# Optimization experiments

Hardware: AMD Instinct MI355X
Metric: run time of the kernel (lower is better)

The kernel has to match this reference:

```python
import jax, jax.numpy as jnp
import numpy as np

N = 100000      # nodes
E = 3200000     # directed edges
G = 1024        # graphs in batch


def setup_inputs() -> dict:
    key = jax.random.key(0)
    ks = jax.random.split(key, 12)
    x = jax.random.normal(ks[0], (N, 4), dtype=jnp.float32)
    edge_index = jax.random.randint(ks[1], (2, E), 0, N, dtype=jnp.int64)
    batch = jnp.sort(jax.random.randint(ks[2], (N,), 0, G, dtype=jnp.int64))
    s = 0.1
    return {
        'x': x, 'edge_index': edge_index, 'batch': batch,
        'W_emb': jax.random.normal(ks[3], (4, 1), jnp.float32) * s,
        'b_emb': jax.random.normal(ks[4], (4,), jnp.float32) * s,
        'W1': jax.random.normal(ks[5], (16, 7), jnp.float32) * s,
        'b1': jax.random.normal(ks[6], (16,), jnp.float32) * s,
        'W2': jax.random.normal(ks[7], (8, 16), jnp.float32) * s,
        'b2': jax.random.normal(ks[8], (8,), jnp.float32) * s,
        'W3': jax.random.normal(ks[9], (1, 8), jnp.float32) * s,
        'b3': jax.random.normal(ks[10], (1,), jnp.float32) * s,
    }


def _gcn_norm(edge_index, n):
    # add self-loops (PyG GCNConv default)
    loops = jnp.arange(n, dtype=edge_index.dtype)
    row = jnp.concatenate([edge_index[0], loops])  # source
    col = jnp.concatenate([edge_index[1], loops])  # target
    deg = jax.ops.segment_sum(jnp.ones_like(col, dtype=jnp.float32), col, num_segments=n)
    dinv = jnp.where(deg > 0, deg ** -0.5, 0.0)
    norm = dinv[row] * dinv[col]
    return row, col, norm


def _gcn_conv(h, W, b, row, col, norm, n):
    h = h @ W.T                                   # [n, out]
    msg = h[row] * norm[:, None]                  # gather + scale
    out = jax.ops.segment_sum(msg, col, num_segments=n)
    return out + b


def reference(x, edge_index, batch, W_emb, b_emb, W1, b1, W2, b2, W3, b3):
    row, col, norm = _gcn_norm(edge_index, N)
    atoms_vector = x[:, :1]
    atoms_xyz = x[:, 1:]
    one_hot_emb = atoms_vector @ W_emb.T + b_emb          # [N, 4]
    h = jnp.concatenate([one_hot_emb, atoms_xyz], axis=1) # [N, 7]
    h = jnp.tanh(_gcn_conv(h, W1, b1, row, col, norm, N)) # [N, 16]
    # dropout is identity in eval mode
    h = jnp.tanh(_gcn_conv(h, W2, b2, row, col, norm, N)) # [N, 8]
    # scatter-mean readout over graphs
    sums = jax.ops.segment_sum(h, batch, num_segments=G)
    cnts = jax.ops.segment_sum(jnp.ones((h.shape[0],), h.dtype), batch, num_segments=G)
    pooled = sums / jnp.maximum(cnts, 1.0)[:, None]       # [G, 8]
    return pooled @ W3.T + b3                             # [G, 1]
```

## Files before the change

### kernel.cpp

```cpp
#include <hip/hip_runtime.h>
#include <hip/hip_fp16.h>


constexpr int BLK  = 256;
constexpr int NPB  = 256;
constexpr int NBMX = 512;
constexpr int CAPB = 9216;
constexpr int PBLK = 512;
constexpr int CAPS = 6144;
constexpr int EPT  = 12;
constexpr int SBLK = 512;
constexpr int NIT4 = 5;
constexpr float S8 = 64.0f;

__global__ void k_place(const int4* __restrict__ row4, const int4* __restrict__ col4,
                        int* __restrict__ bucketCnt, unsigned int* __restrict__ data,
                        int E, int NB) {
    __shared__ unsigned int stage[CAPS];
    __shared__ unsigned short stageB[CAPS];
    __shared__ int pos[4][NBMX];
    __shared__ int sstart[NBMX], lbase[NBMX];
    __shared__ int wsum[8];
    int t = threadIdx.x;
    int lane = t & 63, w = t >> 6;
    int rep = (lane >> 4) & 3;
    int begin = blockIdx.x * CAPS;
    int end = min(E, begin + CAPS);
    int csize = end - begin;
    int q0 = begin >> 2, q1 = end >> 2;
#pragma unroll
    for (int rr = 0; rr < 4; rr++) pos[rr][t] = 0;
    __syncthreads();
    unsigned int ent[EPT];
    int meta[EPT];
#pragma unroll
    for (int it = 0; it < EPT / 4; it++) {
        int i = q0 + t + it * PBLK;
        bool ok = i < q1;
        int4 c = ok ? col4[i] : make_int4(0, 0, 0, 0);
        int4 r = ok ? row4[i] : make_int4(0, 0, 0, 0);
#pragma unroll
        for (int k = 0; k < 4; k++) {
            int cc = ((const int*)&c)[k];
            int rr = ((const int*)&r)[k];
            int b = cc >> 8;
            int o = ok ? atomicAdd(&pos[rep][b], 1) : 0;
            ent[it * 4 + k] = ((unsigned int)(cc & 255) << 17) | (unsigned int)rr;
            meta[it * 4 + k] = ok ? ((rep << 22) | (b << 13) | o) : -1;
        }
    }
    __syncthreads();
    int p0 = pos[0][t], p1 = pos[1][t], p2 = pos[2][t], p3 = pos[3][t];
    int v = p0 + p1 + p2 + p3;
    int sc = v;
#pragma unroll
    for (int off = 1; off < 64; off <<= 1) {
        int o = __shfl_up(sc, off, 64);
        if (lane >= off) sc += o;
    }
    if (lane == 63) wsum[w] = sc;
    __syncthreads();
    int pre = 0;
#pragma unroll
    for (int i = 0; i < 8; i++) if (i < w) pre += wsum[i];
    int excl = sc + pre - v;
    sstart[t] = excl;
    lbase[t] = v ? atomicAdd(&bucketCnt[t], v) : 0;
    pos[0][t] = 0;
    pos[1][t] = p0;
    pos[2][t] = p0 + p1;
    pos[3][t] = p0 + p1 + p2;
    __syncthreads();
#pragma unroll
    for (int k = 0; k < EPT; k++) {
        int m = meta[k];
        if (m >= 0) {
            int rr = m >> 22;
            int b  = (m >> 13) & 0x1FF;
            int o  = m & 0x1FFF;
            int idx = sstart[b] + pos[rr][b] + o;
            stage[idx]  = ent[k];
            stageB[idx] = (unsigned short)b;
        }
    }
    __syncthreads();
    for (int k = t; k < csize; k += PBLK) {
        int b = stageB[k];
        data[(unsigned int)b * CAPB + (unsigned int)(lbase[b] + (k - sstart[b]))] = stage[k];
    }
}

__global__ void k_sort_node1(unsigned int* __restrict__ data,
                             const int* __restrict__ bucketCnt,
                             const float4* __restrict__ x,
                             const float* __restrict__ Wemb, const float* __restrict__ bemb,
                             const float* __restrict__ W1,
                             int* __restrict__ rs, int* __restrict__ re,
                             float* __restrict__ dinv, uint4* __restrict__ u1q, int n) {
    __shared__ int pos[8][NPB], startl[NPB];
    __shared__ int wsum[4];
    int b = blockIdx.x;
    int t = threadIdx.x;
    int lane = t & 63;
    int rep = (lane >> 3) & 7;
    int base = b * CAPB;
    int cnt = min(bucketCnt[b], CAPB);
#pragma unroll
    for (int z = 0; z < 4; z++) ((int*)pos)[t + z * SBLK] = 0;
    __syncthreads();
    const uint4* data4 = (const uint4*)(data + base);
    unsigned int ent[NIT4 * 4];
    int off[NIT4 * 4];
#pragma unroll
    for (int it = 0; it < NIT4; it++) {
        int i4 = t + it * SBLK;
        int i = i4 * 4;
        uint4 p4 = (i < cnt) ? data4[i4] : make_uint4(0, 0, 0, 0);
#pragma unroll
        for (int k = 0; k < 4; k++) {
            int idx = it * 4 + k;
            if (i + k < cnt) {
                unsigned int p = ((const unsigned int*)&p4)[k];
                int dloc = (int)(p >> 17);
                int o = atomicAdd(&pos[rep][dloc], 1);
                ent[idx] = p & 0x1FFFF;
                off[idx] = (rep << 22) | (dloc << 14) | o;
            } else off[idx] = -1;
        }
    }
    __syncthreads();
    int node = b * NPB + t;
    float d = 0.0f;
    if (t < NPB) {
        int w = t >> 6;
        int p[8];
        int v = 0;
#pragma unroll
        for (int r = 0; r < 8; r++) { p[r] = pos[r][t]; v += p[r]; }
        int sc = v;
#pragma unroll
        for (int o = 1; o < 64; o <<= 1) {
            int s = __shfl_up(sc, o, 64);
            if (lane >= o) sc += s;
        }
        if (lane == 63) wsum[w] = sc;
        __syncthreads();
        int pre = 0;
#pragma unroll
        for (int i = 0; i < 4; i++) if (i < w) pre += wsum[i];
        int excl = sc + pre - v;
        startl[t] = excl;
        int run = 0;
#pragma unroll
        for (int r = 0; r < 8; r++) { pos[r][t] = run; run += p[r]; }
        if (node < n) {
            rs[node] = base + excl;
            re[node] = base + excl + v;
            d = rsqrtf((float)v + 1.0f);
            dinv[node] = d;
        }
    } else {
        __syncthreads();
    }
    __syncthreads();
#pragma unroll
    for (int it = 0; it < NIT4 * 4; it++) {
        int m = off[it];
        if (m >= 0) {
            int rr = (m >> 22) & 7;
            int dl = (m >> 14) & 255;
            int o  = m & 0x3FFF;
            data[base + startl[dl] + pos[rr][dl] + o] = ent[it];
        }
    }
    if (t < NPB && node < n) {
        float4 xi = x[node];
        float h0[7];
#pragma unroll
        for (int j = 0; j < 4; j++) h0[j] = xi.x * Wemb[j] + bemb[j];
        h0[4] = xi.y; h0[5] = xi.z; h0[6] = xi.w;
        float s[16];
#pragma unroll
        for (int f = 0; f < 16; f++) {
            float tt = 0.0f;
#pragma unroll
            for (int j = 0; j < 7; j++) tt += h0[j] * W1[f * 7 + j];
            s[f] = tt * d * S8;
        }
        unsigned int w0, w1, w2, w3;
        w0 = __builtin_amdgcn_cvt_pk_fp8_f32(s[0],  s[1],  0,  false);
        w0 = __builtin_amdgcn_cvt_pk_fp8_f32(s[2],  s[3],  w0, true);
        w1 = __builtin_amdgcn_cvt_pk_fp8_f32(s[4],  s[5],  0,  false);
        w1 = __builtin_amdgcn_cvt_pk_fp8_f32(s[6],  s[7],  w1, true);
        w2 = __builtin_amdgcn_cvt_pk_fp8_f32(s[8],  s[9],  0,  false);
        w2 = __builtin_amdgcn_cvt_pk_fp8_f32(s[10], s[11], w2, true);
        w3 = __builtin_amdgcn_cvt_pk_fp8_f32(s[12], s[13], 0,  false);
        w3 = __builtin_amdgcn_cvt_pk_fp8_f32(s[14], s[15], w3, true);
        u1q[node] = make_uint4(w0, w1, w2, w3);
    }
}

typedef float vfloat2 __attribute__((vector_size(8)));

__device__ __forceinline__ void dec16_add(uint4 q, float* acc) {
#pragma unroll
    for (int w = 0; w < 4; w++) {
        unsigned int u = ((const unsigned int*)&q)[w];
        vfloat2 lo = __builtin_amdgcn_cvt_pk_f32_fp8(u, false);
        vfloat2 hi = __builtin_amdgcn_cvt_pk_f32_fp8(u, true);
        acc[4 * w + 0] += lo[0]; acc[4 * w + 1] += lo[1];
        acc[4 * w + 2] += hi[0]; acc[4 * w + 3] += hi[1];
    }
}

__global__ void k_agg1(const unsigned int* __restrict__ sorted,
                       const int* __restrict__ rs, const int* __restrict__ re,
                       const uint4* __restrict__ u1q, const float* __restrict__ dinv,
                       const float* __restrict__ b1, const float* __restrict__ W2,
                       uint4* __restrict__ u2q, int n) {
    int tt = blockIdx.x * BLK + threadIdx.x;
    int node = tt >> 2;
    int j = tt & 3;
    if (node >= n) return;
    int s = rs[node], e = re[node];
    float d = dinv[node];
    uint4 qs = make_uint4(0, 0, 0, 0);
    if (j == 0) qs = u1q[node];
    float acc[16];
#pragma unroll
    for (int k = 0; k < 16; k++) acc[k] = 0.0f;
    int i = s + j;
    for (; i + 12 < e; i += 16) {
        uint4 q0 = u1q[sorted[i]];
        uint4 q1 = u1q[sorted[i + 4]];
        uint4 q2 = u1q[sorted[i + 8]];
        uint4 q3 = u1q[sorted[i + 12]];
        dec16_add(q0, acc);
        dec16_add(q1, acc);
        dec16_add(q2, acc);
        dec16_add(q3, acc);
    }
    for (; i + 4 < e; i += 8) {
        uint4 q0 = u1q[sorted[i]];
        uint4 q1 = u1q[sorted[i + 4]];
        dec16_add(q0, acc);
        dec16_add(q1, acc);
    }
    if (i < e) {
        uint4 q = u1q[sorted[i]];
        dec16_add(q, acc);
    }
    if (j == 0) dec16_add(qs, acc);
#pragma unroll
    for (int k = 0; k < 16; k++) {
        acc[k] += __shfl_xor(acc[k], 1, 64);
        acc[k] += __shfl_xor(acc[k], 2, 64);
    }
    float dS = d * (1.0f / S8);
    float h1[16];
#pragma unroll
    for (int k = 0; k < 16; k++) h1[k] = tanhf(dS * acc[k] + b1[k]);
    float r[8];
#pragma unroll
    for (int g = 0; g < 8; g++) {
        float ttv = 0.0f;
#pragma unroll
        for (int k = 0; k < 16; k++) ttv += h1[k] * W2[g * 16 + k];
        r[g] = ttv * d;
    }
    if (j == 0) {
        union { __half2 h2[4]; uint4 u4; } pk;
#pragma unroll
        for (int q = 0; q < 4; q++) pk.h2[q] = __floats2half2_rn(r[2 * q], r[2 * q + 1]);
        u2q[node] = pk.u4;
    }
}

__device__ __forceinline__ void h16_add(uint4 q, float* acc) {
    const __half2* p = (const __half2*)&q;
#pragma unroll
    for (int k = 0; k < 4; k++) {
        float2 a = __half22float2(p[k]);
        acc[2 * k]     += a.x;
        acc[2 * k + 1] += a.y;
    }
}

__global__ void k_agg2_pool(const unsigned int* __restrict__ sorted,
                            const int* __restrict__ rs, const int* __restrict__ re,
                            const uint4* __restrict__ u2q, const float* __restrict__ dinv,
                            const float* __restrict__ b2, const int* __restrict__ batch,
                            float* __restrict__ pooled, float* __restrict__ cnt, int n) {
    int tt = blockIdx.x * BLK + threadIdx.x;
    int node = tt >> 2;
    int j = tt & 3;
    int lane = threadIdx.x & 63;
    bool valid = node < n;
    float h[8];
#pragma unroll
    for (int k = 0; k < 8; k++) h[k] = 0.0f;
    int g = -1;
    float c = 0.0f;
    if (valid) {
        int s = rs[node], e = re[node];
        float d = dinv[node];
        uint4 qs = make_uint4(0, 0, 0, 0);
        int gq = 0;
        if (j == 0) {
            qs = u2q[node];
            gq = batch[node];
        }
        float acc[8];
#pragma unroll
        for (int k = 0; k < 8; k++) acc[k] = 0.0f;
        int i = s + j;
        for (; i + 12 < e; i += 16) {
            uint4 q0 = u2q[sorted[i]];
            uint4 q1 = u2q[sorted[i + 4]];
            uint4 q2 = u2q[sorted[i + 8]];
            uint4 q3 = u2q[sorted[i + 12]];
            h16_add(q0, acc);
            h16_add(q1, acc);
            h16_add(q2, acc);
            h16_add(q3, acc);
        }
        for (; i + 4 < e; i += 8) {
            uint4 q0 = u2q[sorted[i]];
            uint4 q1 = u2q[sorted[i + 4]];
            h16_add(q0, acc);
            h16_add(q1, acc);
        }
        if (i < e) {
            uint4 q = u2q[sorted[i]];
            h16_add(q, acc);
        }
        if (j == 0) h16_add(qs, acc);
#pragma unroll
        for (int k = 0; k < 8; k++) {
            acc[k] += __shfl_xor(acc[k], 1, 64);
            acc[k] += __shfl_xor(acc[k], 2, 64);
        }
        if (j == 0) {
#pragma unroll
            for (int k = 0; k < 8; k++) h[k] = tanhf(d * acc[k] + b2[k]);
            g = gq;
            c = 1.0f;
        }
    }
#pragma unroll
    for (int off = 4; off < 64; off <<= 1) {
        int gn = __shfl_down(g, off, 64);
        float cn = __shfl_down(c, off, 64);
        float hn[8];
#pragma unroll
        for (int k = 0; k < 8; k++) hn[k] = __shfl_down(h[k], off, 64);
        bool take = (lane + off < 64) && (gn == g);
        if (take) {
            c += cn;
#pragma unroll
            for (int k = 0; k < 8; k++) h[k] += hn[k];
        }
    }
    int gprev = __shfl_up(g, 4, 64);
    bool head = valid && (j == 0) && (lane == 0 || gprev != g);
    if (head) {
#pragma unroll
        for (int k = 0; k < 8; k++) atomicAdd(&pooled[g * 8 + k], h[k]);
        atomicAdd(&cnt[g], c);
    }
}

__global__ void k_out(const float* __restrict__ pooled, const float* __restrict__ cnt,
                      const float* __restrict__ W3, const float* __restrict__ b3,
                      float* __restrict__ out, int G) {
    int g = blockIdx.x * BLK + threadIdx.x;
    if (g >= G) return;
    float c = fmaxf(cnt[g], 1.0f);
    float t = 0.0f;
#pragma unroll
    for (int k = 0; k < 8; k++) t += pooled[g * 8 + k] * W3[k];
    out[g] = t / c + b3[0];
}

extern "C" void kernel_launch(void* const* d_in, const int* in_sizes, int n_in,
                              void* d_out, int out_size, void* d_ws, size_t ws_size,
                              hipStream_t stream) {
    const float* x    = (const float*)d_in[0];
    const int*   ei   = (const int*)d_in[1];
    const int*   batch= (const int*)d_in[2];
    const float* Wemb = (const float*)d_in[3];
    const float* bemb = (const float*)d_in[4];
    const float* W1   = (const float*)d_in[5];
    const float* b1   = (const float*)d_in[6];
    const float* W2   = (const float*)d_in[7];
    const float* b2   = (const float*)d_in[8];
    const float* W3   = (const float*)d_in[9];
    const float* b3   = (const float*)d_in[10];
    float* out = (float*)d_out;

    const int n = in_sizes[2];
    const int E = in_sizes[1] / 2;
    const int G = out_size;
    const int* row = ei;
    const int* col = ei + E;
    const int NB = (n + NPB - 1) / NPB;

    float* ws    = (float*)d_ws;
    float* dinv  = ws;
    uint4* u1q   = (uint4*)(ws + n);
    __half* u2h  = (__half*)(ws + 9 * n);
    int* rs      = (int*)(ws + 13 * n);
    int* re      = rs + n;
    int* bucketCnt = re + n;
    float* pooled  = (float*)(bucketCnt + NBMX);
    float* cnt     = pooled + 8 * G;
    unsigned int* data = (unsigned int*)(cnt + G);

    int gridP = (E + CAPS - 1) / CAPS;
    int gridA = (4 * n + BLK - 1) / BLK;

    hipMemsetAsync(bucketCnt, 0, (NBMX + 8 * G + G) * sizeof(int), stream);
    k_place<<<gridP, PBLK, 0, stream>>>((const int4*)row, (const int4*)col,
                                        bucketCnt, data, E, NB);
    k_sort_node1<<<NB, SBLK, 0, stream>>>(data, bucketCnt, (const float4*)x,
                                          Wemb, bemb, W1, rs, re, dinv, u1q, n);
    k_agg1<<<gridA, BLK, 0, stream>>>(data, rs, re, u1q,
                                      dinv, b1, W2, (uint4*)u2h, n);
    k_agg2_pool<<<gridA, BLK, 0, stream>>>(data, rs, re,
                                           (const uint4*)u2h, dinv, b2,
                                           batch, pooled, cnt, n);
    k_out<<<(G + BLK - 1) / BLK, BLK, 0, stream>>>(pooled, cnt, W3, b3, out, G);
}
```

Measured before the change: 180.3 us.

## Replace bucketed two-pass CSR sort with global atomic histogram and scatter

Replaces the LDS-staged bucket placement and per-bucket local sort with a plain counting sort: a global atomic degree histogram, a per-block scan that claims row offsets through an atomic cursor, and an atomic-cursor scatter of source indices into CSR order. This drops the shared-memory staging and the capacity-bounded bucket layout, so the code is simpler and no longer has a per-bucket overflow limit. In exchange it issues millions of global atomics on random addresses plus random scattered writes, and edge order within a row becomes nondeterministic. Blocks claim row ranges through the cursor in arbitrary order, so node ranges are no longer laid out in node order.

New measurement: 536.3 us. 2.97x slower.

```diff
diff --git a/kernel.cpp b/kernel.cpp
--- a/kernel.cpp
+++ b/kernel.cpp
@@ -3,201 +3,92 @@
 
 
 constexpr int BLK  = 256;
-constexpr int NPB  = 256;
-constexpr int NBMX = 512;
-constexpr int CAPB = 9216;
-constexpr int PBLK = 512;
-constexpr int CAPS = 6144;
-constexpr int EPT  = 12;
-constexpr int SBLK = 512;
-constexpr int NIT4 = 5;
 constexpr float S8 = 64.0f;
 
-__global__ void k_place(const int4* __restrict__ row4, const int4* __restrict__ col4,
-                        int* __restrict__ bucketCnt, unsigned int* __restrict__ data,
-                        int E, int NB) {
-    __shared__ unsigned int stage[CAPS];
-    __shared__ unsigned short stageB[CAPS];
-    __shared__ int pos[4][NBMX];
-    __shared__ int sstart[NBMX], lbase[NBMX];
-    __shared__ int wsum[8];
+__global__ void k_hist(const int4* __restrict__ col4, int* __restrict__ deg, int nq) {
+    int i = blockIdx.x * BLK + threadIdx.x;
+    if (i >= nq) return;
+    int4 c = col4[i];
+    atomicAdd(&deg[c.x], 1);
+    atomicAdd(&deg[c.y], 1);
+    atomicAdd(&deg[c.z], 1);
+    atomicAdd(&deg[c.w], 1);
+}
+
+__global__ void k_node1(const int* __restrict__ deg,
+                        const float4* __restrict__ x,
+                        const float* __restrict__ Wemb, const float* __restrict__ bemb,
+                        const float* __restrict__ W1,
+                        int* __restrict__ rs, int* __restrict__ re,
+                        int* __restrict__ cur, float* __restrict__ dinv,
+                        uint4* __restrict__ u1q, int* __restrict__ bucketCursor, int n) {
+    __shared__ int wsum[4];
+    __shared__ int sbase;
     int t = threadIdx.x;
+    int node = blockIdx.x * BLK + t;
     int lane = t & 63, w = t >> 6;
-    int rep = (lane >> 4) & 3;
-    int begin = blockIdx.x * CAPS;
-    int end = min(E, begin + CAPS);
-    int csize = end - begin;
-    int q0 = begin >> 2, q1 = end >> 2;
-#pragma unroll
-    for (int rr = 0; rr < 4; rr++) pos[rr][t] = 0;
-    __syncthreads();
-    unsigned int ent[EPT];
-    int meta[EPT];
-#pragma unroll
-    for (int it = 0; it < EPT / 4; it++) {
-        int i = q0 + t + it * PBLK;
-        bool ok = i < q1;
-        int4 c = ok ? col4[i] : make_int4(0, 0, 0, 0);
-        int4 r = ok ? row4[i] : make_int4(0, 0, 0, 0);
-#pragma unroll
-        for (int k = 0; k < 4; k++) {
-            int cc = ((const int*)&c)[k];
-            int rr = ((const int*)&r)[k];
-            int b = cc >> 8;
-            int o = ok ? atomicAdd(&pos[rep][b], 1) : 0;
-            ent[it * 4 + k] = ((unsigned int)(cc & 255) << 17) | (unsigned int)rr;
-            meta[it * 4 + k] = ok ? ((rep << 22) | (b << 13) | o) : -1;
-        }
-    }
-    __syncthreads();
-    int p0 = pos[0][t], p1 = pos[1][t], p2 = pos[2][t], p3 = pos[3][t];
-    int v = p0 + p1 + p2 + p3;
+    int v = (node < n) ? deg[node] : 0;
     int sc = v;
 #pragma unroll
-    for (int off = 1; off < 64; off <<= 1) {
-        int o = __shfl_up(sc, off, 64);
-        if (lane >= off) sc += o;
+    for (int o = 1; o < 64; o <<= 1) {
+        int s = __shfl_up(sc, o, 64);
+        if (lane >= o) sc += s;
     }
     if (lane == 63) wsum[w] = sc;
     __syncthreads();
     int pre = 0;
 #pragma unroll
-    for (int i = 0; i < 8; i++) if (i < w) pre += wsum[i];
-    int excl = sc + pre - v;
-    sstart[t] = excl;
-    lbase[t] = v ? atomicAdd(&bucketCnt[t], v) : 0;
-    pos[0][t] = 0;
-    pos[1][t] = p0;
-    pos[2][t] = p0 + p1;
-    pos[3][t] = p0 + p1 + p2;
+    for (int i = 0; i < 4; i++) if (i < w) pre += wsum[i];
+    int excl = pre + sc - v;
+    int total = wsum[0] + wsum[1] + wsum[2] + wsum[3];
+    if (t == 0) sbase = atomicAdd(bucketCursor, total);
     __syncthreads();
-#pragma unroll
-    for (int k = 0; k < EPT; k++) {
-        int m = meta[k];
-        if (m >= 0) {
-            int rr = m >> 22;
-            int b  = (m >> 13) & 0x1FF;
-            int o  = m & 0x1FFF;
-            int idx = sstart[b] + pos[rr][b] + o;
-            stage[idx]  = ent[k];
-            stageB[idx] = (unsigned short)b;
-        }
-    }
-    __syncthreads();
-    for (int k = t; k < csize; k += PBLK) {
-        int b = stageB[k];
-        data[(unsigned int)b * CAPB + (unsigned int)(lbase[b] + (k - sstart[b]))] = stage[k];
-    }
-}
-
-__global__ void k_sort_node1(unsigned int* __restrict__ data,
-                             const int* __restrict__ bucketCnt,
-                             const float4* __restrict__ x,
-                             const float* __restrict__ Wemb, const float* __restrict__ bemb,
-                             const float* __restrict__ W1,
-                             int* __restrict__ rs, int* __restrict__ re,
-                             float* __restrict__ dinv, uint4* __restrict__ u1q, int n) {
-    __shared__ int pos[8][NPB], startl[NPB];
-    __shared__ int wsum[4];
-    int b = blockIdx.x;
-    int t = threadIdx.x;
-    int lane = t & 63;
-    int rep = (lane >> 3) & 7;
-    int base = b * CAPB;
-    int cnt = min(bucketCnt[b], CAPB);
-#pragma unroll
-    for (int z = 0; z < 4; z++) ((int*)pos)[t + z * SBLK] = 0;
-    __syncthreads();
-    const uint4* data4 = (const uint4*)(data + base);
-    unsigned int ent[NIT4 * 4];
-    int off[NIT4 * 4];
-#pragma unroll
-    for (int it = 0; it < NIT4; it++) {
-        int i4 = t + it * SBLK;
-        int i = i4 * 4;
-        uint4 p4 = (i < cnt) ? data4[i4] : make_uint4(0, 0, 0, 0);
-#pragma unroll
-        for (int k = 0; k < 4; k++) {
-            int idx = it * 4 + k;
-            if (i + k < cnt) {
-                unsigned int p = ((const unsigned int*)&p4)[k];
-                int dloc = (int)(p >> 17);
-                int o = atomicAdd(&pos[rep][dloc], 1);
-                ent[idx] = p & 0x1FFFF;
-                off[idx] = (rep << 22) | (dloc << 14) | o;
-            } else off[idx] = -1;
-        }
-    }
-    __syncthreads();
-    int node = b * NPB + t;
-    float d = 0.0f;
-    if (t < NPB) {
-        int w = t >> 6;
-        int p[8];
-        int v = 0;
-#pragma unroll
-        for (int r = 0; r < 8; r++) { p[r] = pos[r][t]; v += p[r]; }
-        int sc = v;
-#pragma unroll
-        for (int o = 1; o < 64; o <<= 1) {
-            int s = __shfl_up(sc, o, 64);
-            if (lane >= o) sc += s;
-        }
-        if (lane == 63) wsum[w] = sc;
-        __syncthreads();
-        int pre = 0;
-#pragma unroll
-        for (int i = 0; i < 4; i++) if (i < w) pre += wsum[i];
-        int excl = sc + pre - v;
-        startl[t] = excl;
-        int run = 0;
-#pragma unroll
-        for (int r = 0; r < 8; r++) { pos[r][t] = run; run += p[r]; }
-        if (node < n) {
-            rs[node] = base + excl;
-            re[node] = base + excl + v;
-            d = rsqrtf((float)v + 1.0f);
-            dinv[node] = d;
-        }
-    } else {
-        __syncthreads();
-    }
-    __syncthreads();
-#pragma unroll
-    for (int it = 0; it < NIT4 * 4; it++) {
-        int m = off[it];
-        if (m >= 0) {
-            int rr = (m >> 22) & 7;
-            int dl = (m >> 14) & 255;
-            int o  = m & 0x3FFF;
-            data[base + startl[dl] + pos[rr][dl] + o] = ent[it];
-        }
-    }
-    if (t < NPB && node < n) {
-        float4 xi = x[node];
-        float h0[7];
-#pragma unroll
-        for (int j = 0; j < 4; j++) h0[j] = xi.x * Wemb[j] + bemb[j];
-        h0[4] = xi.y; h0[5] = xi.z; h0[6] = xi.w;
-        float s[16];
-#pragma unroll
-        for (int f = 0; f < 16; f++) {
-            float tt = 0.0f;
-#pragma unroll
-            for (int j = 0; j < 7; j++) tt += h0[j] * W1[f * 7 + j];
-            s[f] = tt * d * S8;
-        }
-        unsigned int w0, w1, w2, w3;
-        w0 = __builtin_amdgcn_cvt_pk_fp8_f32(s[0],  s[1],  0,  false);
-        w0 = __builtin_amdgcn_cvt_pk_fp8_f32(s[2],  s[3],  w0, true);
-        w1 = __builtin_amdgcn_cvt_pk_fp8_f32(s[4],  s[5],  0,  false);
-        w1 = __builtin_amdgcn_cvt_pk_fp8_f32(s[6],  s[7],  w1, true);
-        w2 = __builtin_amdgcn_cvt_pk_fp8_f32(s[8],  s[9],  0,  false);
-        w2 = __builtin_amdgcn_cvt_pk_fp8_f32(s[10], s[11], w2, true);
-        w3 = __builtin_amdgcn_cvt_pk_fp8_f32(s[12], s[13], 0,  false);
-        w3 = __builtin_amdgcn_cvt_pk_fp8_f32(s[14], s[15], w3, true);
-        u1q[node] = make_uint4(w0, w1, w2, w3);
-    }
+    if (node >= n) return;
+    int r0 = sbase + excl;
+    rs[node] = r0;
+    re[node] = r0 + v;
+    cur[node] = r0;
+    float d = rsqrtf((float)v + 1.0f);
+    dinv[node] = d;
+    float4 xi = x[node];
+    float h0[7];
+#pragma unroll
+    for (int j = 0; j < 4; j++) h0[j] = xi.x * Wemb[j] + bemb[j];
+    h0[4] = xi.y; h0[5] = xi.z; h0[6] = xi.w;
+    float s[16];
+#pragma unroll
+    for (int f = 0; f < 16; f++) {
+        float tt = 0.0f;
+#pragma unroll
+        for (int j = 0; j < 7; j++) tt += h0[j] * W1[f * 7 + j];
+        s[f] = tt * d * S8;
+    }
+    unsigned int w0, w1, w2, w3;
+    w0 = __builtin_amdgcn_cvt_pk_fp8_f32(s[0],  s[1],  0,  false);
+    w0 = __builtin_amdgcn_cvt_pk_fp8_f32(s[2],  s[3],  w0, true);
+    w1 = __builtin_amdgcn_cvt_pk_fp8_f32(s[4],  s[5],  0,  false);
+    w1 = __builtin_amdgcn_cvt_pk_fp8_f32(s[6],  s[7],  w1, true);
+    w2 = __builtin_amdgcn_cvt_pk_fp8_f32(s[8],  s[9],  0,  false);
+    w2 = __builtin_amdgcn_cvt_pk_fp8_f32(s[10], s[11], w2, true);
+    w3 = __builtin_amdgcn_cvt_pk_fp8_f32(s[12], s[13], 0,  false);
+    w3 = __builtin_amdgcn_cvt_pk_fp8_f32(s[14], s[15], w3, true);
+    u1q[node] = make_uint4(w0, w1, w2, w3);
+}
+
+__global__ void k_scatter(const int4* __restrict__ row4, const int4* __restrict__ col4,
+                          int* __restrict__ cur, unsigned int* __restrict__ data, int nq) {
+    int i = blockIdx.x * BLK + threadIdx.x;
+    if (i >= nq) return;
+    int4 r = row4[i];
+    int4 c = col4[i];
+    int p0 = atomicAdd(&cur[c.x], 1);
+    int p1 = atomicAdd(&cur[c.y], 1);
+    int p2 = atomicAdd(&cur[c.z], 1);
+    int p3 = atomicAdd(&cur[c.w], 1);
+    data[p0] = (unsigned int)r.x;
+    data[p1] = (unsigned int)r.y;
+    data[p2] = (unsigned int)r.z;
+    data[p3] = (unsigned int)r.w;
 }
 
 typedef float vfloat2 __attribute__((vector_size(8)));
@@ -403,7 +294,6 @@
     const int G = out_size;
     const int* row = ei;
     const int* col = ei + E;
-    const int NB = (n + NPB - 1) / NPB;
 
     float* ws    = (float*)d_ws;
     float* dinv  = ws;
@@ -411,19 +301,24 @@
     __half* u2h  = (__half*)(ws + 9 * n);
     int* rs      = (int*)(ws + 13 * n);
     int* re      = rs + n;
-    int* bucketCnt = re + n;
-    float* pooled  = (float*)(bucketCnt + NBMX);
+    int* cur     = re + n;
+    int* deg     = cur + n;
+    int* bucketCursor = deg + n;
+    float* pooled  = (float*)(bucketCursor + 64);
     float* cnt     = pooled + 8 * G;
     unsigned int* data = (unsigned int*)(cnt + G);
 
-    int gridP = (E + CAPS - 1) / CAPS;
+    int nq    = E / 4;
+    int gridQ = (nq + BLK - 1) / BLK;
+    int gridN = (n + BLK - 1) / BLK;
     int gridA = (4 * n + BLK - 1) / BLK;
 
-    hipMemsetAsync(bucketCnt, 0, (NBMX + 8 * G + G) * sizeof(int), stream);
-    k_place<<<gridP, PBLK, 0, stream>>>((const int4*)row, (const int4*)col,
-                                        bucketCnt, data, E, NB);
-    k_sort_node1<<<NB, SBLK, 0, stream>>>(data, bucketCnt, (const float4*)x,
-                                          Wemb, bemb, W1, rs, re, dinv, u1q, n);
+    hipMemsetAsync(deg, 0, (n + 64 + 9 * G) * sizeof(int), stream);
+    k_hist<<<gridQ, BLK, 0, stream>>>((const int4*)col, deg, nq);
+    k_node1<<<gridN, BLK, 0, stream>>>(deg, (const float4*)x, Wemb, bemb, W1,
+                                       rs, re, cur, dinv, u1q, bucketCursor, n);
+    k_scatter<<<gridQ, BLK, 0, stream>>>((const int4*)row, (const int4*)col,
+                                         cur, data, nq);
     k_agg1<<<gridA, BLK, 0, stream>>>(data, rs, re, u1q,
                                       dinv, b1, W2, (uint4*)u2h, n);
     k_agg2_pool<<<gridA, BLK, 0, stream>>>(data, rs, re,
```
